# Optimization experiments

Hardware: AMD Instinct MI355X
Metric: run time of the kernel (lower is better)

## Reference

```python
import jax, jax.numpy as jnp
import numpy as np

EPS = 1e-5  # torch InstanceNorm2d default eps

def conv1x1(x, w, b):
    # x: [B,C,H,W], w: [O,C], b: [O]
    return jnp.einsum('bchw,oc->bohw', x, w) + b[None, :, None, None]

def instance_norm(x):
    # InstanceNorm2d(affine=False): normalize per-sample, per-channel over H,W
    mean = jnp.mean(x, axis=(2, 3), keepdims=True)
    var = jnp.var(x, axis=(2, 3), keepdims=True)
    return (x - mean) * jax.lax.rsqrt(var + EPS)

def proj(x, w, b):
    return jax.nn.relu(instance_norm(conv1x1(x, w, b)))

def setup_inputs() -> dict:
    key = jax.random.key(0)
    ks = jax.random.split(key, 9)
    B, C, Ci, H, W = 16, 256, 128, 64, 64
    s_in = 1.0 / np.sqrt(C)
    s_mid = 1.0 / np.sqrt(Ci)
    return {
        'x': jax.random.normal(ks[0], (B, C, H, W), jnp.float32),
        'g_w': jax.random.normal(ks[1], (Ci, C), jnp.float32) * s_in,
        'g_b': jax.random.normal(ks[2], (Ci,), jnp.float32) * s_in,
        'theta_w': jax.random.normal(ks[3], (Ci, C), jnp.float32) * s_in,
        'theta_b': jax.random.normal(ks[4], (Ci,), jnp.float32) * s_in,
        'phi_w': jax.random.normal(ks[5], (Ci, C), jnp.float32) * s_in,
        'phi_b': jax.random.normal(ks[6], (Ci,), jnp.float32) * s_in,
        'W_w': jax.random.normal(ks[7], (C, Ci), jnp.float32) * s_mid,
        'W_b': jax.random.normal(ks[8], (C,), jnp.float32) * s_mid,
    }

def reference(x, g_w, g_b, theta_w, theta_b, phi_w, phi_b, W_w, W_b):
    B, C, H, W = x.shape
    Ci = g_w.shape[0]
    N = H * W
    g_x = proj(x, g_w, g_b).reshape(B, Ci, N)        # [B,Ci,N]
    theta_x = proj(x, theta_w, theta_b).reshape(B, Ci, N)
    phi_x = proj(x, phi_w, phi_b).reshape(B, Ci, N)
    # channel-attention Gram matrix [B,Ci,Ci], softmax over last dim
    f = jnp.einsum('bin,bjn->bij', theta_x, phi_x)
    attn = jax.nn.softmax(f, axis=2)
    y = jnp.einsum('bij,bjn->bin', attn, g_x)        # [B,Ci,N]
    # replicate torch permute(0,2,1).contiguous().view(B,Ci,H,W)
    y = jnp.transpose(y, (0, 2, 1)).reshape(B, Ci, H, W)
    y = instance_norm(conv1x1(y, W_w, W_b))
    return y + x
```

## Files before the change

### kernel.cpp

```cpp
#include <hip/hip_runtime.h>

#define DEVINL __device__ __forceinline__

typedef __attribute__((ext_vector_type(8))) _Float16 h8v;
typedef __attribute__((ext_vector_type(4))) float f32x4;
typedef __attribute__((ext_vector_type(8))) unsigned short us8;
typedef __attribute__((ext_vector_type(4))) unsigned short us4;

DEVINL unsigned short f2h(float f) {
  return __builtin_bit_cast(unsigned short, (_Float16)f);
}
DEVINL float h2f(unsigned short u) {
  return (float)__builtin_bit_cast(_Float16, u);
}

__global__ __launch_bounds__(256)
void prep_weights(const float* __restrict__ g_w, const float* __restrict__ th_w,
                  const float* __restrict__ ph_w, const float* __restrict__ W_w,
                  unsigned short* __restrict__ wall_h, unsigned short* __restrict__ wall_l,
                  unsigned short* __restrict__ w2h)
{
  const int i = blockIdx.x * 256 + threadIdx.x;
  float v;
  if (i < 32768) v = th_w[i];
  else if (i < 65536) v = ph_w[i - 32768];
  else v = g_w[i - 65536];
  const unsigned short h = f2h(v);
  wall_h[i] = h;
  if (i < 65536) wall_l[i] = f2h(v - h2f(h));
  if (i < 32768) w2h[i] = f2h(W_w[i]);
}

__global__ __launch_bounds__(512, 2)
void proj_gemm(const unsigned short* __restrict__ wall_h,
               const unsigned short* __restrict__ wall_l,
               const float* __restrict__ x,
               float* __restrict__ zr, unsigned short* __restrict__ zg,
               float* __restrict__ partials)
{
  __shared__ __align__(16) unsigned short smem[64512];
  unsigned short* As_h = smem;
  unsigned short* As_l = smem + 27648;
  unsigned short* Bs_h = smem + 46080;
  unsigned short* Bs_l = smem + 55296;

  const int t = threadIdx.x;
  const int lane = t & 63;
  const int wave = t >> 6;
  const int wm = wave >> 1, wn = wave & 1;
  const int lr = lane & 15, lk = lane >> 4;
  const int b = blockIdx.z;
  const int bx = blockIdx.x;
  const int nbase = bx * 128;
  const float* xs = x + (long)b * 256 * 4096;

  f32x4 acc[6][4];
#pragma unroll
  for (int i = 0; i < 6; ++i)
#pragma unroll
    for (int j = 0; j < 4; ++j) acc[i][j] = (f32x4)0.0f;

  const int nl = t & 127, cg = t >> 7;

  for (int kt = 0; kt < 4; ++kt) {
    const int k0 = kt * 64;
#pragma unroll
    for (int i = 0; i < 6; ++i) {
      const int q = i * 512 + t;
      const int row = q >> 3, c = q & 7;
      *(us8*)&As_h[row * 72 + c * 8] = *(const us8*)&wall_h[(long)row * 256 + k0 + c * 8];
    }
#pragma unroll
    for (int i = 0; i < 4; ++i) {
      const int q = i * 512 + t;
      const int row = q >> 3, c = q & 7;
      *(us8*)&As_l[row * 72 + c * 8] = *(const us8*)&wall_l[(long)row * 256 + k0 + c * 8];
    }
#pragma unroll
    for (int hp = 0; hp < 2; ++hp) {
      float xv[8];
#pragma unroll
      for (int i = 0; i < 8; ++i)
        xv[i] = xs[(long)(k0 + cg * 16 + hp * 8 + i) * 4096 + nbase + nl];
      us8 h8, l8;
#pragma unroll
      for (int e = 0; e < 8; ++e) {
        const unsigned short hb = f2h(xv[e]);
        h8[e] = hb;
        l8[e] = f2h(xv[e] - h2f(hb));
      }
      *(us8*)&Bs_h[nl * 72 + cg * 16 + hp * 8] = h8;
      *(us8*)&Bs_l[nl * 72 + cg * 16 + hp * 8] = l8;
    }
    __syncthreads();

#pragma unroll
    for (int ks = 0; ks < 2; ++ks) {
      const int ko = ks * 32 + lk * 8;
      h8v bh[4], bl[4];
#pragma unroll
      for (int ni = 0; ni < 4; ++ni) {
        const int r = (wn * 64 + ni * 16 + lr) * 72 + ko;
        bh[ni] = *(const h8v*)&Bs_h[r];
        bl[ni] = *(const h8v*)&Bs_l[r];
      }
#pragma unroll
      for (int mi = 0; mi < 6; ++mi) {
        const int fr = mi * 4 + wm;
        const h8v ah = *(const h8v*)&As_h[(fr * 16 + lr) * 72 + ko];
        if (fr < 16) {
          const h8v al = *(const h8v*)&As_l[(fr * 16 + lr) * 72 + ko];
#pragma unroll
          for (int ni = 0; ni < 4; ++ni) {
            acc[mi][ni] = __builtin_amdgcn_mfma_f32_16x16x32_f16(bh[ni], ah, acc[mi][ni], 0, 0, 0);
            acc[mi][ni] = __builtin_amdgcn_mfma_f32_16x16x32_f16(bl[ni], ah, acc[mi][ni], 0, 0, 0);
            acc[mi][ni] = __builtin_amdgcn_mfma_f32_16x16x32_f16(bh[ni], al, acc[mi][ni], 0, 0, 0);
          }
        } else {
#pragma unroll
          for (int ni = 0; ni < 4; ++ni)
            acc[mi][ni] = __builtin_amdgcn_mfma_f32_16x16x32_f16(bh[ni], ah, acc[mi][ni], 0, 0, 0);
        }
      }
    }
    __syncthreads();
  }

  float* sbuf = (float*)smem;
#pragma unroll
  for (int mi = 0; mi < 6; ++mi) {
    float s = 0.f, ss = 0.f;
#pragma unroll
    for (int ni = 0; ni < 4; ++ni)
#pragma unroll
      for (int r = 0; r < 4; ++r) {
        const float v = acc[mi][ni][r];
        s += v; ss += v * v;
      }
    const int fr = mi * 4 + wm;
    const int slot = ((fr * 16 + lr) * 8 + (wn * 4 + lk)) * 2;
    sbuf[slot] = s; sbuf[slot + 1] = ss;
  }
  __syncthreads();
  if (t < 384) {
    float s = 0.f, ss = 0.f;
#pragma unroll
    for (int w = 0; w < 8; ++w) {
      s += sbuf[(t * 8 + w) * 2];
      ss += sbuf[(t * 8 + w) * 2 + 1];
    }
    const long pidx = ((long)bx * 6144 + b * 384 + t) * 2;
    partials[pidx] = s; partials[pidx + 1] = ss;
  }

#pragma unroll
  for (int mi = 0; mi < 6; ++mi)
#pragma unroll
    for (int ni = 0; ni < 4; ++ni) {
      const int gm = (mi * 4 + wm) * 16 + lr;
      const int gn = nbase + wn * 64 + ni * 16 + lk * 4;
      if (mi < 4) {
        *(f32x4*)&zr[((long)b * 256 + gm) * 4096 + gn] = acc[mi][ni];
      } else {
        us4 hv;
#pragma unroll
        for (int r = 0; r < 4; ++r) hv[r] = f2h(acc[mi][ni][r]);
        *(us4*)&zg[((long)b * 128 + (gm - 256)) * 4096 + gn] = hv;
      }
    }
}

__global__ __launch_bounds__(256)
void stats_reduce(const float* __restrict__ partials, float* __restrict__ stats)
{
  const int row = blockIdx.x * 256 + threadIdx.x;
  float s = 0.f, ss = 0.f;
#pragma unroll
  for (int k = 0; k < 32; ++k) {
    s += partials[((long)k * 6144 + row) * 2];
    ss += partials[((long)k * 6144 + row) * 2 + 1];
  }
  const float mean = s * (1.f / 4096.f);
  const float var = ss * (1.f / 4096.f) - mean * mean;
  const float rs = rsqrtf(fmaxf(var, 0.f) + 1e-5f);
  stats[row * 2] = rs;
  stats[row * 2 + 1] = -mean * rs;
}

__global__ __launch_bounds__(256, 2)
void fgemm_norm(const float* __restrict__ zr,
                const float* __restrict__ stats, float* __restrict__ fpart)
{
  __shared__ __align__(16) unsigned short As_h[128 * 72];
  __shared__ __align__(16) unsigned short As_l[128 * 72];
  __shared__ __align__(16) unsigned short Bs_h[128 * 72];
  __shared__ __align__(16) unsigned short Bs_l[128 * 72];

  const int t = threadIdx.x;
  const int lane = t & 63;
  const int wave = t >> 6;
  const int wm = wave >> 1, wn = wave & 1;
  const int lr = lane & 15, lk = lane >> 4;
  const int zb = blockIdx.z >> 5, z1 = blockIdx.z & 31;
  const int koff = z1 * 128;

  f32x4 acc[4][4];
#pragma unroll
  for (int i = 0; i < 4; ++i)
#pragma unroll
    for (int j = 0; j < 4; ++j) acc[i][j] = (f32x4)0.0f;

  for (int kt = 0; kt < 2; ++kt) {
    const int k0 = koff + kt * 64;
#pragma unroll
    for (int i = 0; i < 4; ++i) {
      const int q = i * 256 + t;
      const int row = q >> 3, c = q & 7;
#pragma unroll
      for (int op = 0; op < 2; ++op) {
        const int zrow = op * 128 + row;
        const float* src = zr + ((long)zb * 256 + zrow) * 4096 + k0 + c * 8;
        const f32x4 v0 = *(const f32x4*)&src[0];
        const f32x4 v1 = *(const f32x4*)&src[4];
        const int srow = zb * 384 + zrow;
        const float rs = stats[srow * 2];
        const float nmrs = stats[srow * 2 + 1];
        us8 oh, ol;
#pragma unroll
        for (int e = 0; e < 8; ++e) {
          const float v = (e < 4) ? v0[e] : v1[e - 4];
          const float nv = fmaxf(__builtin_fmaf(v, rs, nmrs), 0.f);
          const unsigned short hb = f2h(nv);
          oh[e] = hb;
          ol[e] = f2h(nv - h2f(hb));
        }
        unsigned short* dh = op ? Bs_h : As_h;
        unsigned short* dl = op ? Bs_l : As_l;
        *(us8*)&dh[row * 72 + c * 8] = oh;
        *(us8*)&dl[row * 72 + c * 8] = ol;
      }
    }
    __syncthreads();
#pragma unroll
    for (int ks = 0; ks < 2; ++ks) {
      const int ko = ks * 32 + lk * 8;
      h8v ah[4], bh[4], al[4], bl[4];
#pragma unroll
      for (int mi = 0; mi < 4; ++mi) {
        const int r = (wm * 64 + mi * 16 + lr) * 72 + ko;
        ah[mi] = *(const h8v*)&As_h[r];
        al[mi] = *(const h8v*)&As_l[r];
      }
#pragma unroll
      for (int ni = 0; ni < 4; ++ni) {
        const int r = (wn * 64 + ni * 16 + lr) * 72 + ko;
        bh[ni] = *(const h8v*)&Bs_h[r];
        bl[ni] = *(const h8v*)&Bs_l[r];
      }
#pragma unroll
      for (int mi = 0; mi < 4; ++mi)
#pragma unroll
        for (int ni = 0; ni < 4; ++ni) {
          acc[mi][ni] = __builtin_amdgcn_mfma_f32_16x16x32_f16(bh[ni], ah[mi], acc[mi][ni], 0, 0, 0);
          acc[mi][ni] = __builtin_amdgcn_mfma_f32_16x16x32_f16(bl[ni], ah[mi], acc[mi][ni], 0, 0, 0);
          acc[mi][ni] = __builtin_amdgcn_mfma_f32_16x16x32_f16(bh[ni], al[mi], acc[mi][ni], 0, 0, 0);
        }
    }
    __syncthreads();
  }

  const long cOff = ((long)zb * 32 + z1) * 16384;
#pragma unroll
  for (int mi = 0; mi < 4; ++mi)
#pragma unroll
    for (int ni = 0; ni < 4; ++ni) {
      const int gm = wm * 64 + mi * 16 + lr;
      const int gn = wn * 64 + ni * 16 + lk * 4;
      *(f32x4*)&fpart[cOff + (long)gm * 128 + gn] = acc[mi][ni];
    }
}

__global__ __launch_bounds__(256, 2)
void gemm_y(const unsigned short* __restrict__ Ah0, const unsigned short* __restrict__ Bh0,
            unsigned short* __restrict__ Cout,
            int lda, int ldb, int ldc, int ksteps, int z1count,
            long aS1, long aS2, long bS1, long bS2, long cS1, long cS2)
{
  __shared__ __align__(16) unsigned short smem[18432];
  unsigned short* As = smem;
  unsigned short* Bs = smem + 9216;

  const int t = threadIdx.x;
  const int lane = t & 63;
  const int wave = t >> 6;
  const int wm = wave >> 1, wn = wave & 1;
  const int lr = lane & 15, lk = lane >> 4;

  const int z = blockIdx.z;
  const int zb = z / z1count, z1 = z - zb * z1count;
  const unsigned short* Ah = Ah0 + zb * aS2 + z1 * aS1;
  const unsigned short* Bh = Bh0 + zb * bS2 + z1 * bS1;
  const long cOff = zb * cS2 + z1 * cS1;

  f32x4 acc[4][4];
#pragma unroll
  for (int i = 0; i < 4; ++i)
#pragma unroll
    for (int j = 0; j < 4; ++j) acc[i][j] = (f32x4)0.0f;

  for (int kt = 0; kt < ksteps; ++kt) {
    const int k0 = kt * 64;
#pragma unroll
    for (int i = 0; i < 4; ++i) {
      const int q = i * 256 + t;
      const int row = q >> 3, c = q & 7;
      const int lo = row * 72 + c * 8;
      *(us8*)&As[lo] = *(const us8*)&Ah[(long)row * lda + k0 + c * 8];
      *(us8*)&Bs[lo] = *(const us8*)&Bh[(long)row * ldb + k0 + c * 8];
    }
    __syncthreads();
#pragma unroll
    for (int ks = 0; ks < 2; ++ks) {
      const int ko = ks * 32 + lk * 8;
      h8v ah[4], bh[4];
#pragma unroll
      for (int mi = 0; mi < 4; ++mi)
        ah[mi] = *(const h8v*)&As[(wm * 64 + mi * 16 + lr) * 72 + ko];
#pragma unroll
      for (int ni = 0; ni < 4; ++ni)
        bh[ni] = *(const h8v*)&Bs[(wn * 64 + ni * 16 + lr) * 72 + ko];
#pragma unroll
      for (int mi = 0; mi < 4; ++mi)
#pragma unroll
        for (int ni = 0; ni < 4; ++ni)
          acc[mi][ni] = __builtin_amdgcn_mfma_f32_16x16x32_f16(bh[ni], ah[mi], acc[mi][ni], 0, 0, 0);
    }
    __syncthreads();
  }

  unsigned short* T = smem;
#pragma unroll
  for (int mi = 0; mi < 4; ++mi)
#pragma unroll
    for (int ni = 0; ni < 4; ++ni) {
      const int gm = wm * 64 + mi * 16 + lr;
      const int gn = wn * 64 + ni * 16 + lk * 4;
      us4 o;
#pragma unroll
      for (int r = 0; r < 4; ++r) o[r] = f2h(acc[mi][ni][r]);
      *(us4*)&T[gm * 132 + gn] = o;
    }
  __syncthreads();
#pragma unroll
  for (int i = 0; i < 8; ++i) {
    const int q = i * 256 + t;
    const int row = q >> 4, c = q & 15;
    const us8 v = *(const us8*)&T[row * 132 + c * 8];
    *(us8*)&Cout[cOff + (long)row * ldc + c * 8] = v;
  }
}

__global__ __launch_bounds__(256, 2)
void conv2_gemm(const unsigned short* __restrict__ w2h,
                const unsigned short* __restrict__ y4T,
                unsigned short* __restrict__ z2b)
{
  __shared__ __align__(16) unsigned short smem[23040];
  unsigned short* As = smem;
  unsigned short* Bs = smem + 18432;

  const int t = threadIdx.x;
  const int lane = t & 63;
  const int wave = t >> 6;
  const int wm = wave;
  const int lr = lane & 15, lk = lane >> 4;
  const int b = blockIdx.z;
  const int nbase = blockIdx.x * 64;
  const unsigned short* Bh = y4T + (long)b * 4096 * 128 + (long)nbase * 128;

  f32x4 acc[4][4];
#pragma unroll
  for (int i = 0; i < 4; ++i)
#pragma unroll
    for (int j = 0; j < 4; ++j) acc[i][j] = (f32x4)0.0f;

  for (int kt = 0; kt < 2; ++kt) {
    const int k0 = kt * 64;
#pragma unroll
    for (int i = 0; i < 8; ++i) {
      const int q = i * 256 + t;
      const int row = q >> 3, c = q & 7;
      *(us8*)&As[row * 72 + c * 8] = *(const us8*)&w2h[(long)row * 128 + k0 + c * 8];
    }
#pragma unroll
    for (int i = 0; i < 2; ++i) {
      const int q = i * 256 + t;
      const int row = q >> 3, c = q & 7;
      *(us8*)&Bs[row * 72 + c * 8] = *(const us8*)&Bh[(long)row * 128 + k0 + c * 8];
    }
    __syncthreads();
#pragma unroll
    for (int ks = 0; ks < 2; ++ks) {
      const int ko = ks * 32 + lk * 8;
      h8v ah[4], bh[4];
#pragma unroll
      for (int mi = 0; mi < 4; ++mi)
        ah[mi] = *(const h8v*)&As[(wm * 64 + mi * 16 + lr) * 72 + ko];
#pragma unroll
      for (int ni = 0; ni < 4; ++ni)
        bh[ni] = *(const h8v*)&Bs[(ni * 16 + lr) * 72 + ko];
#pragma unroll
      for (int mi = 0; mi < 4; ++mi)
#pragma unroll
        for (int ni = 0; ni < 4; ++ni)
          acc[mi][ni] = __builtin_amdgcn_mfma_f32_16x16x32_f16(bh[ni], ah[mi], acc[mi][ni], 0, 0, 0);
    }
    __syncthreads();
  }

  unsigned short* T = smem;
#pragma unroll
  for (int mi = 0; mi < 4; ++mi)
#pragma unroll
    for (int ni = 0; ni < 4; ++ni) {
      const int gm = wm * 64 + mi * 16 + lr;
      const int gn = ni * 16 + lk * 4;
      us4 o;
#pragma unroll
      for (int r = 0; r < 4; ++r) o[r] = f2h(acc[mi][ni][r]);
      *(us4*)&T[gm * 72 + gn] = o;
    }
  __syncthreads();
#pragma unroll
  for (int i = 0; i < 8; ++i) {
    const int q = i * 256 + t;
    const int row = q >> 3, c = q & 7;
    const us8 v = *(const us8*)&T[row * 72 + c * 8];
    *(us8*)&z2b[((long)b * 256 + row) * 4096 + nbase + c * 8] = v;
  }
}

__global__ __launch_bounds__(256)
void norm_transpose_g(const unsigned short* __restrict__ zg,
                      const float* __restrict__ stats,
                      unsigned short* __restrict__ gT)
{
  __shared__ unsigned short T[64 * 136];
  const int b = blockIdx.y, n0 = blockIdx.x * 64;
  const int t = threadIdx.x;
  const int c = t >> 1, part = t & 1;
  const int grow = b * 384 + 256 + c;
  const float rs = stats[grow * 2];
  const float nmrs = stats[grow * 2 + 1];
  const long off = ((long)b * 128 + c) * 4096 + n0 + part * 32;
#pragma unroll
  for (int j = 0; j < 4; ++j) {
    const us8 h = *(const us8*)&zg[off + j * 8];
#pragma unroll
    for (int e = 0; e < 8; ++e) {
      const float nv = fmaxf(__builtin_fmaf(h2f(h[e]), rs, nmrs), 0.f);
      T[(part * 32 + j * 8 + e) * 136 + c] = f2h(nv);
    }
  }
  __syncthreads();
  const int nl = t >> 2, q = t & 3;
  const long obase = ((long)b * 4096 + n0 + nl) * 128 + q * 32;
#pragma unroll
  for (int k = 0; k < 4; ++k) {
    us8 o;
#pragma unroll
    for (int e = 0; e < 8; ++e) o[e] = T[nl * 136 + q * 32 + k * 8 + e];
    *(us8*)&gT[obase + k * 8] = o;
  }
}

__global__ __launch_bounds__(256)
void softmax_attn(const float* __restrict__ fpart, unsigned short* __restrict__ attn)
{
  const int row = blockIdx.x * 4 + (threadIdx.x >> 6);
  const int b = row >> 7, i = row & 127;
  const int t = threadIdx.x & 63;
  float v0 = 0.f, v1 = 0.f;
#pragma unroll
  for (int kc = 0; kc < 32; ++kc) {
    const float* p = fpart + ((long)(b * 32 + kc)) * 16384 + i * 128;
    v0 += p[t];
    v1 += p[t + 64];
  }
  float mx = fmaxf(v0, v1);
  for (int o = 32; o > 0; o >>= 1) mx = fmaxf(mx, __shfl_xor(mx, o));
  const float e0 = __expf(v0 - mx), e1 = __expf(v1 - mx);
  float s = e0 + e1;
  for (int o = 32; o > 0; o >>= 1) s += __shfl_xor(s, o);
  const float inv = 1.f / s;
  attn[(long)row * 128 + t] = f2h(e0 * inv);
  attn[(long)row * 128 + t + 64] = f2h(e1 * inv);
}

__global__ __launch_bounds__(256)
void finalize(const unsigned short* __restrict__ z2b, const float* __restrict__ x,
              float* __restrict__ out)
{
  const int row = blockIdx.x;
  const long base = (long)row * 4096;
  const int t = threadIdx.x;
  float v[16];
  float s = 0.f, ss = 0.f;
#pragma unroll
  for (int h = 0; h < 2; ++h) {
    us8 u = *(const us8*)&z2b[base + t * 16 + h * 8];
#pragma unroll
    for (int e = 0; e < 8; ++e) {
      const float f = h2f(u[e]);
      v[h * 8 + e] = f;
      s += f; ss += f * f;
    }
  }
  __shared__ float r0[256], r1[256];
  r0[t] = s; r1[t] = ss;
  __syncthreads();
  for (int o = 128; o > 0; o >>= 1) {
    if (t < o) { r0[t] += r0[t + o]; r1[t] += r1[t + o]; }
    __syncthreads();
  }
  const float mean = r0[0] * (1.f / 4096.f);
  const float var = r1[0] * (1.f / 4096.f) - mean * mean;
  const float rs = rsqrtf(fmaxf(var, 0.f) + 1e-5f);
#pragma unroll
  for (int i = 0; i < 4; ++i) {
    f32x4 xr = *(const f32x4*)&x[base + t * 16 + i * 4];
    f32x4 o;
#pragma unroll
    for (int e = 0; e < 4; ++e) o[e] = (v[i * 4 + e] - mean) * rs + xr[e];
    *(f32x4*)&out[base + t * 16 + i * 4] = o;
  }
}

extern "C" void kernel_launch(void* const* d_in, const int* in_sizes, int n_in,
                              void* d_out, int out_size, void* d_ws, size_t ws_size,
                              hipStream_t stream)
{
  const float* x    = (const float*)d_in[0];
  const float* g_w  = (const float*)d_in[1];
  const float* th_w = (const float*)d_in[3];
  const float* ph_w = (const float*)d_in[5];
  const float* W_w  = (const float*)d_in[7];

  char* ws = (char*)d_ws;
  const size_t MB = 1024ull * 1024ull;
  if (ws_size < 186 * MB) return;

  float*          zr       = (float*)(ws);
  unsigned short* zg       = (unsigned short*)(ws + 64 * MB);
  float*          fpart    = (float*)(ws + 80 * MB);
  unsigned short* attn     = (unsigned short*)(ws + 112 * MB);
  unsigned short* gT       = (unsigned short*)(ws + 113 * MB);
  unsigned short* y4T      = (unsigned short*)(ws + 129 * MB);
  unsigned short* z2b      = (unsigned short*)(ws);
  float*          partials = (float*)(ws + 145 * MB);
  float*          stats    = (float*)(ws + 149 * MB);
  unsigned short* wall_h   = (unsigned short*)(ws + 150 * MB);
  unsigned short* wall_l   = (unsigned short*)(ws + 150 * MB + 256 * 1024);
  unsigned short* w2h      = (unsigned short*)(ws + 150 * MB + 512 * 1024);

  prep_weights<<<dim3(384), 256, 0, stream>>>(g_w, th_w, ph_w, W_w, wall_h, wall_l, w2h);

  proj_gemm<<<dim3(32, 1, 16), 512, 0, stream>>>(wall_h, wall_l, x, zr, zg, partials);

  stats_reduce<<<dim3(24), 256, 0, stream>>>(partials, stats);

  norm_transpose_g<<<dim3(64, 16), 256, 0, stream>>>(zg, stats, gT);

  fgemm_norm<<<dim3(1, 1, 512), 256, 0, stream>>>(zr, stats, fpart);

  softmax_attn<<<dim3(512), 256, 0, stream>>>(fpart, attn);

  gemm_y<<<dim3(1, 1, 512), 256, 0, stream>>>(
      attn, gT, y4T,
      128, 4096, 128, 2, 32,
      0, 16384, 128, (long)4096 * 128, 16384, (long)4096 * 128);

  conv2_gemm<<<dim3(64, 1, 16), 256, 0, stream>>>(w2h, y4T, z2b);

  finalize<<<dim3(4096), 256, 0, stream>>>(z2b, x, (float*)d_out);
}
```

Baseline: 148.4 us.

## Prefetch next x tile into registers and stage weights via direct global-to-LDS loads

```diff
diff --git a/kernel.cpp b/kernel.cpp
--- a/kernel.cpp
+++ b/kernel.cpp
@@ -13,6 +13,12 @@
 DEVINL float h2f(unsigned short u) {
   return (float)__builtin_bit_cast(_Float16, u);
 }
+
+#if __has_builtin(__builtin_amdgcn_global_load_lds)
+#define HAVE_GLOAD_LDS 1
+#else
+#define HAVE_GLOAD_LDS 0
+#endif
 
 __global__ __launch_bounds__(256)
 void prep_weights(const float* __restrict__ g_w, const float* __restrict__ th_w,
@@ -62,37 +68,90 @@
 
   const int nl = t & 127, cg = t >> 7;
 
+  float xv[16];
+
+#define STAGE_A(K0)                                                              \
+  do {                                                                           \
+    _STAGE_A_IMPL(K0)                                                            \
+  } while (0)
+
+#if HAVE_GLOAD_LDS
+#define _STAGE_A_IMPL(K0)                                                        \
+  _Pragma("unroll")                                                              \
+  for (int i_ = 0; i_ < 7; ++i_) {                                               \
+    const int ch = i_ * 8 + wave;                                                \
+    if (ch < 54) {                                                               \
+      const int s = ch * 512 + (lane << 3);                                      \
+      const int row = s / 72;                                                    \
+      const int c8 = (s - row * 72) >> 3;                                        \
+      const unsigned short* src =                                                \
+          (c8 < 8) ? &wall_h[(long)row * 256 + (K0) + c8 * 8] : wall_h;          \
+      __builtin_amdgcn_global_load_lds(                                          \
+          (const __attribute__((address_space(1))) unsigned int*)src,            \
+          (__attribute__((address_space(3))) unsigned int*)&As_h[ch * 512],      \
+          16, 0, 0);                                                             \
+    }                                                                            \
+  }                                                                              \
+  _Pragma("unroll")                                                              \
+  for (int i_ = 0; i_ < 5; ++i_) {                                               \
+    const int ch = i_ * 8 + wave;                                                \
+    if (ch < 36) {                                                               \
+      const int s = ch * 512 + (lane << 3);                                      \
+      const int row = s / 72;                                                    \
+      const int c8 = (s - row * 72) >> 3;                                        \
+      const unsigned short* src =                                                \
+          (c8 < 8) ? &wall_l[(long)row * 256 + (K0) + c8 * 8] : wall_l;          \
+      __builtin_amdgcn_global_load_lds(                                          \
+          (const __attribute__((address_space(1))) unsigned int*)src,            \
+          (__attribute__((address_space(3))) unsigned int*)&As_l[ch * 512],      \
+          16, 0, 0);                                                             \
+    }                                                                            \
+  }
+#else
+#define _STAGE_A_IMPL(K0)                                                        \
+  _Pragma("unroll")                                                              \
+  for (int i_ = 0; i_ < 6; ++i_) {                                               \
+    const int q = i_ * 512 + t;                                                  \
+    const int row = q >> 3, c = q & 7;                                           \
+    *(us8*)&As_h[row * 72 + c * 8] =                                             \
+        *(const us8*)&wall_h[(long)row * 256 + (K0) + c * 8];                    \
+  }                                                                              \
+  _Pragma("unroll")                                                              \
+  for (int i_ = 0; i_ < 4; ++i_) {                                               \
+    const int q = i_ * 512 + t;                                                  \
+    const int row = q >> 3, c = q & 7;                                           \
+    *(us8*)&As_l[row * 72 + c * 8] =                                             \
+        *(const us8*)&wall_l[(long)row * 256 + (K0) + c * 8];                    \
+  }
+#endif
+
+#define LOAD_X(K0)                                                               \
+  _Pragma("unroll")                                                              \
+  for (int i_ = 0; i_ < 16; ++i_)                                                \
+    xv[i_] = xs[(long)((K0) + cg * 16 + i_) * 4096 + nbase + nl];
+
+#define CONV_WRITE_B()                                                           \
+  _Pragma("unroll")                                                              \
+  for (int hp = 0; hp < 2; ++hp) {                                               \
+    us8 h8, l8;                                                                  \
+    _Pragma("unroll")                                                            \
+    for (int e = 0; e < 8; ++e) {                                                \
+      const float v_ = xv[hp * 8 + e];                                           \
+      const unsigned short hb_ = f2h(v_);                                        \
+      h8[e] = hb_;                                                               \
+      l8[e] = f2h(v_ - h2f(hb_));                                                \
+    }                                                                            \
+    *(us8*)&Bs_h[nl * 72 + cg * 16 + hp * 8] = h8;                               \
+    *(us8*)&Bs_l[nl * 72 + cg * 16 + hp * 8] = l8;                               \
+  }
+
+  STAGE_A(0);
+  LOAD_X(0);
+  CONV_WRITE_B();
+  __syncthreads();
+
   for (int kt = 0; kt < 4; ++kt) {
-    const int k0 = kt * 64;
-#pragma unroll
-    for (int i = 0; i < 6; ++i) {
-      const int q = i * 512 + t;
-      const int row = q >> 3, c = q & 7;
-      *(us8*)&As_h[row * 72 + c * 8] = *(const us8*)&wall_h[(long)row * 256 + k0 + c * 8];
-    }
-#pragma unroll
-    for (int i = 0; i < 4; ++i) {
-      const int q = i * 512 + t;
-      const int row = q >> 3, c = q & 7;
-      *(us8*)&As_l[row * 72 + c * 8] = *(const us8*)&wall_l[(long)row * 256 + k0 + c * 8];
-    }
-#pragma unroll
-    for (int hp = 0; hp < 2; ++hp) {
-      float xv[8];
-#pragma unroll
-      for (int i = 0; i < 8; ++i)
-        xv[i] = xs[(long)(k0 + cg * 16 + hp * 8 + i) * 4096 + nbase + nl];
-      us8 h8, l8;
-#pragma unroll
-      for (int e = 0; e < 8; ++e) {
-        const unsigned short hb = f2h(xv[e]);
-        h8[e] = hb;
-        l8[e] = f2h(xv[e] - h2f(hb));
-      }
-      *(us8*)&Bs_h[nl * 72 + cg * 16 + hp * 8] = h8;
-      *(us8*)&Bs_l[nl * 72 + cg * 16 + hp * 8] = l8;
-    }
-    __syncthreads();
+    if (kt < 3) { LOAD_X((kt + 1) * 64); }
 
 #pragma unroll
     for (int ks = 0; ks < 2; ++ks) {
@@ -124,6 +183,12 @@
       }
     }
     __syncthreads();
+
+    if (kt < 3) {
+      STAGE_A((kt + 1) * 64);
+      CONV_WRITE_B();
+      __syncthreads();
+    }
   }
 
   float* sbuf = (float*)smem;
@@ -168,6 +233,10 @@
         *(us4*)&zg[((long)b * 128 + (gm - 256)) * 4096 + gn] = hv;
       }
     }
+#undef STAGE_A
+#undef _STAGE_A_IMPL
+#undef LOAD_X
+#undef CONV_WRITE_B
 }
 
 __global__ __launch_bounds__(256)
```

Result: no change. 148.4 us (-0.0%).

## Double-buffer proj_gemm K loop with direct global-to-LDS weight loads

Applied to the files above, without the earlier changes.

```diff
diff --git a/kernel.cpp b/kernel.cpp
--- a/kernel.cpp
+++ b/kernel.cpp
@@ -13,6 +13,12 @@
 DEVINL float h2f(unsigned short u) {
   return (float)__builtin_bit_cast(_Float16, u);
 }
+
+#if __has_builtin(__builtin_amdgcn_global_load_lds)
+#define HAVE_GLOAD_LDS 1
+#else
+#define HAVE_GLOAD_LDS 0
+#endif
 
 __global__ __launch_bounds__(256)
 void prep_weights(const float* __restrict__ g_w, const float* __restrict__ th_w,
@@ -31,18 +37,14 @@
   if (i < 32768) w2h[i] = f2h(W_w[i]);
 }
 
-__global__ __launch_bounds__(512, 2)
+__global__ __launch_bounds__(512)
 void proj_gemm(const unsigned short* __restrict__ wall_h,
                const unsigned short* __restrict__ wall_l,
                const float* __restrict__ x,
                float* __restrict__ zr, unsigned short* __restrict__ zg,
                float* __restrict__ partials)
 {
-  __shared__ __align__(16) unsigned short smem[64512];
-  unsigned short* As_h = smem;
-  unsigned short* As_l = smem + 27648;
-  unsigned short* Bs_h = smem + 46080;
-  unsigned short* Bs_l = smem + 55296;
+  __shared__ __align__(16) unsigned short smem[71680];
 
   const int t = threadIdx.x;
   const int lane = t & 63;
@@ -62,54 +64,124 @@
 
   const int nl = t & 127, cg = t >> 7;
 
-  for (int kt = 0; kt < 4; ++kt) {
-    const int k0 = kt * 64;
-#pragma unroll
-    for (int i = 0; i < 6; ++i) {
-      const int q = i * 512 + t;
-      const int row = q >> 3, c = q & 7;
-      *(us8*)&As_h[row * 72 + c * 8] = *(const us8*)&wall_h[(long)row * 256 + k0 + c * 8];
-    }
-#pragma unroll
-    for (int i = 0; i < 4; ++i) {
-      const int q = i * 512 + t;
-      const int row = q >> 3, c = q & 7;
-      *(us8*)&As_l[row * 72 + c * 8] = *(const us8*)&wall_l[(long)row * 256 + k0 + c * 8];
-    }
-#pragma unroll
-    for (int hp = 0; hp < 2; ++hp) {
-      float xv[8];
-#pragma unroll
-      for (int i = 0; i < 8; ++i)
-        xv[i] = xs[(long)(k0 + cg * 16 + hp * 8 + i) * 4096 + nbase + nl];
-      us8 h8, l8;
-#pragma unroll
-      for (int e = 0; e < 8; ++e) {
-        const unsigned short hb = f2h(xv[e]);
-        h8[e] = hb;
-        l8[e] = f2h(xv[e] - h2f(hb));
-      }
-      *(us8*)&Bs_h[nl * 72 + cg * 16 + hp * 8] = h8;
-      *(us8*)&Bs_l[nl * 72 + cg * 16 + hp * 8] = l8;
-    }
-    __syncthreads();
-
-#pragma unroll
-    for (int ks = 0; ks < 2; ++ks) {
-      const int ko = ks * 32 + lk * 8;
+  float xva[8], xvb[8];
+
+#if HAVE_GLOAD_LDS
+#define GLOAD_A(K0, BUF)                                                         \
+  do {                                                                           \
+    unsigned short* dsth_ = smem + (BUF) * 25600;                                \
+    unsigned short* dstl_ = dsth_ + 15360;                                       \
+    _Pragma("unroll")                                                            \
+    for (int i_ = 0; i_ < 4; ++i_) {                                             \
+      const int ch = i_ * 8 + wave;                                              \
+      if (ch < 30) {                                                             \
+        const int s = ch * 512 + (lane << 3);                                    \
+        const int row = s / 40;                                                  \
+        const int c8 = (s - row * 40) >> 3;                                      \
+        const unsigned short* src =                                              \
+            (c8 < 4) ? &wall_h[(long)row * 256 + (K0) + c8 * 8] : wall_h;        \
+        __builtin_amdgcn_global_load_lds(                                        \
+            (const __attribute__((address_space(1))) unsigned int*)src,          \
+            (__attribute__((address_space(3))) unsigned int*)&dsth_[ch * 512],   \
+            16, 0, 0);                                                           \
+      }                                                                          \
+    }                                                                            \
+    _Pragma("unroll")                                                            \
+    for (int i_ = 0; i_ < 3; ++i_) {                                             \
+      const int ch = i_ * 8 + wave;                                              \
+      if (ch < 20) {                                                             \
+        const int s = ch * 512 + (lane << 3);                                    \
+        const int row = s / 40;                                                  \
+        const int c8 = (s - row * 40) >> 3;                                      \
+        const unsigned short* src =                                              \
+            (c8 < 4) ? &wall_l[(long)row * 256 + (K0) + c8 * 8] : wall_l;        \
+        __builtin_amdgcn_global_load_lds(                                        \
+            (const __attribute__((address_space(1))) unsigned int*)src,          \
+            (__attribute__((address_space(3))) unsigned int*)&dstl_[ch * 512],   \
+            16, 0, 0);                                                           \
+      }                                                                          \
+    }                                                                            \
+  } while (0)
+#else
+#define GLOAD_A(K0, BUF)                                                         \
+  do {                                                                           \
+    unsigned short* dsth_ = smem + (BUF) * 25600;                                \
+    unsigned short* dstl_ = dsth_ + 15360;                                       \
+    _Pragma("unroll")                                                            \
+    for (int i_ = 0; i_ < 3; ++i_) {                                             \
+      const int q = i_ * 512 + t;                                                \
+      const int row = q >> 2, c = q & 3;                                         \
+      *(us8*)&dsth_[row * 40 + c * 8] =                                          \
+          *(const us8*)&wall_h[(long)row * 256 + (K0) + c * 8];                  \
+    }                                                                            \
+    _Pragma("unroll")                                                            \
+    for (int i_ = 0; i_ < 2; ++i_) {                                             \
+      const int q = i_ * 512 + t;                                                \
+      const int row = q >> 2, c = q & 3;                                         \
+      *(us8*)&dstl_[row * 40 + c * 8] =                                          \
+          *(const us8*)&wall_l[(long)row * 256 + (K0) + c * 8];                  \
+    }                                                                            \
+  } while (0)
+#endif
+
+#define LOAD_X(K0, XV)                                                           \
+  _Pragma("unroll")                                                              \
+  for (int i_ = 0; i_ < 8; ++i_)                                                 \
+    XV[i_] = xs[(long)((K0) + cg * 8 + i_) * 4096 + nbase + nl];
+
+#define CONV_WRITE_B(XV, BUF)                                                    \
+  do {                                                                           \
+    unsigned short* bh_ = smem + 51200 + (BUF) * 10240;                          \
+    unsigned short* bl_ = bh_ + 5120;                                            \
+    us8 h8_, l8_;                                                                \
+    _Pragma("unroll")                                                            \
+    for (int e = 0; e < 8; ++e) {                                                \
+      const float v_ = XV[e];                                                    \
+      const unsigned short hb_ = f2h(v_);                                        \
+      h8_[e] = hb_;                                                              \
+      l8_[e] = f2h(v_ - h2f(hb_));                                               \
+    }                                                                            \
+    *(us8*)&bh_[nl * 40 + cg * 8] = h8_;                                         \
+    *(us8*)&bl_[nl * 40 + cg * 8] = l8_;                                         \
+  } while (0)
+
+  LOAD_X(0, xva);
+  GLOAD_A(0, 0);
+  CONV_WRITE_B(xva, 0);
+  LOAD_X(32, xvb);
+  __syncthreads();
+
+#pragma unroll
+  for (int kt = 0; kt < 8; ++kt) {
+    const int cur = kt & 1, nxt = cur ^ 1;
+    if (kt < 7) GLOAD_A((kt + 1) * 32, nxt);
+    if (kt & 1) {
+      if (kt < 7) CONV_WRITE_B(xva, nxt);
+      if (kt < 6) LOAD_X((kt + 2) * 32, xvb);
+    } else {
+      if (kt < 7) CONV_WRITE_B(xvb, nxt);
+      if (kt < 6) LOAD_X((kt + 2) * 32, xva);
+    }
+
+    {
+      const unsigned short* Ah = smem + cur * 25600;
+      const unsigned short* Al = Ah + 15360;
+      const unsigned short* Bh = smem + 51200 + cur * 10240;
+      const unsigned short* Bl = Bh + 5120;
+      const int ko = lk * 8;
       h8v bh[4], bl[4];
 #pragma unroll
       for (int ni = 0; ni < 4; ++ni) {
-        const int r = (wn * 64 + ni * 16 + lr) * 72 + ko;
-        bh[ni] = *(const h8v*)&Bs_h[r];
-        bl[ni] = *(const h8v*)&Bs_l[r];
+        const int r = (wn * 64 + ni * 16 + lr) * 40 + ko;
+        bh[ni] = *(const h8v*)&Bh[r];
+        bl[ni] = *(const h8v*)&Bl[r];
       }
 #pragma unroll
       for (int mi = 0; mi < 6; ++mi) {
         const int fr = mi * 4 + wm;
-        const h8v ah = *(const h8v*)&As_h[(fr * 16 + lr) * 72 + ko];
+        const h8v ah = *(const h8v*)&Ah[(fr * 16 + lr) * 40 + ko];
         if (fr < 16) {
-          const h8v al = *(const h8v*)&As_l[(fr * 16 + lr) * 72 + ko];
+          const h8v al = *(const h8v*)&Al[(fr * 16 + lr) * 40 + ko];
 #pragma unroll
           for (int ni = 0; ni < 4; ++ni) {
             acc[mi][ni] = __builtin_amdgcn_mfma_f32_16x16x32_f16(bh[ni], ah, acc[mi][ni], 0, 0, 0);
@@ -168,6 +240,9 @@
         *(us4*)&zg[((long)b * 128 + (gm - 256)) * 4096 + gn] = hv;
       }
     }
+#undef GLOAD_A
+#undef LOAD_X
+#undef CONV_WRITE_B
 }
 
 __global__ __launch_bounds__(256)
```

Result: slower. 152.6 us (+2.8%).
